# Kernel optimization log

Measured on AMD Instinct MI355X. Metric: run time of the kernel, lower is better.

The kernel has to match this reference:

```python
import jax, jax.numpy as jnp
import numpy as np

B, T, D, H = 4, 256, 256, 4
D2 = 2 * D
DH = D2 // H
SCALE = float(D) ** -0.5


def _swish(x):
    return x * jax.nn.sigmoid(x)


def setup_inputs():
    key = jax.random.key(0)
    ks = jax.random.split(key, 16)

    def w(k, shape, fan_in):
        return jax.random.normal(k, shape, dtype=jnp.float32) / np.float32(np.sqrt(fan_in))

    return {
        "x": jax.random.normal(ks[0], (B, T, D), dtype=jnp.float32),
        "ln_g": jnp.ones((D,), jnp.float32), "ln_b": jnp.zeros((D,), jnp.float32),
        "W_left": w(ks[1], (D2, D), D), "b_left": jnp.zeros((D2,), jnp.float32),
        "W_right": w(ks[2], (D2, D), D), "b_right": jnp.zeros((D2,), jnp.float32),
        "Wi": w(ks[3], (1, D2), D2), "bi": jnp.zeros((1,), jnp.float32),
        "Wf": w(ks[4], (1, D2), D2), "bf": jnp.zeros((1,), jnp.float32),
        "Wo": w(ks[5], (D2, D2), D2), "bo": jnp.zeros((D2,), jnp.float32),
        "Wq": w(ks[6], (H, DH, DH), DH),
        "Wk": w(ks[7], (H, DH, DH), DH),
        "Wv": w(ks[8], (H, DH, DH), DH),
        "conv_w": w(ks[9], (D2, D2, 4), D2 * 4), "conv_b": jnp.zeros((D2,), jnp.float32),
        "skip_W": w(ks[10], (D2, D2), D2),
        "gn_g": jnp.ones((D2,), jnp.float32), "gn_b": jnp.zeros((D2,), jnp.float32),
        "W_last": w(ks[11], (D, D2), D2), "b_last": jnp.zeros((D,), jnp.float32),
    }


def reference(x, ln_g, ln_b, W_left, b_left, W_right, b_right, Wi, bi, Wf, bf,
              Wo, bo, Wq, Wk, Wv, conv_w, conv_b, skip_W, gn_g, gn_b, W_last, b_last):
    # LayerNorm over last dim (eps=1e-5, torch default)
    mu = x.mean(-1, keepdims=True)
    var = x.var(-1, keepdims=True)
    x_norm = (x - mu) * jax.lax.rsqrt(var + 1e-5) * ln_g + ln_b

    x_left = x_norm @ W_left.T + b_left          # (B,T,D2)
    x_right = x_norm @ W_right.T + b_right       # (B,T,D2)

    # causal conv1d: kernel 4, left pad 3
    xc = jnp.transpose(x_left, (0, 2, 1))        # (B,C,T)
    yc = jax.lax.conv_general_dilated(xc, conv_w, (1,), [(3, 0)],
                                      dimension_numbers=("NCH", "OIH", "NCH"))
    x_trans = _swish(jnp.transpose(yc + conv_b[None, :, None], (0, 2, 1)))  # (B,T,D2)

    def bd(z, W):  # block-diagonal linear, W: (H, out_h, in_h)
        zr = z.reshape(B, T, H, DH)
        return jnp.einsum("bthi,hoi->btho", zr, W).reshape(B, T, D2)

    # precompute all per-step projections (hoist GEMMs out of the scan)
    i_bar = x_left @ Wi.T + bi                   # (B,T,1)
    f_bar = x_left @ Wf.T + bf                   # (B,T,1)
    o = jax.nn.sigmoid(x_left @ Wo.T + bo)       # (B,T,D2)
    q = bd(x_trans, Wq)
    k = SCALE * bd(x_trans, Wk)
    v = bd(x_left, Wv)

    xs = tuple(jnp.swapaxes(a, 0, 1) for a in (i_bar, f_bar, q, k, v))  # (T,B,...)
    c0 = jnp.zeros((B, D2, D2), x.dtype)
    n0 = jnp.zeros((B, D2), x.dtype)
    m0 = jnp.zeros((B, 1), x.dtype)

    def step(carry, xs_t):
        c, n, m = carry
        ib, fb, qt, kt, vt = xs_t
        m_next = jnp.maximum(fb + m, ib)
        i_g = jnp.exp(ib - m_next)               # (B,1)
        f_g = jnp.exp(fb + m - m_next)           # (B,1)
        c_next = f_g[..., None] * c + i_g[..., None] * (vt[:, :, None] * kt[:, None, :])
        n_next = f_g * n + i_g * kt
        cq = jnp.einsum("bde,be->bd", c_next, qt)
        denom = jnp.maximum(jnp.abs(jnp.sum(n_next * qt, -1, keepdims=True)), 1.0)
        return (c_next, n_next, m_next), cq / (denom + 1e-8)

    _, h_bar = jax.lax.scan(step, (c0, n0, m0), xs)
    h_seq = o * jnp.swapaxes(h_bar, 0, 1)        # (B,T,D2), output gate applied per step

    # GroupNorm on (B, C, T): normalize per (batch, group) over C/G and T
    z = h_seq.reshape(B, T, H, DH)
    mu_g = z.mean(axis=(1, 3), keepdims=True)
    var_g = z.var(axis=(1, 3), keepdims=True)
    zn = ((z - mu_g) * jax.lax.rsqrt(var_g + 1e-5)).reshape(B, T, D2)
    h_gn = zn * gn_g + gn_b + x_trans @ skip_W.T

    h = h_gn * _swish(x_right)
    return h @ W_last.T + b_last + x
```

## Files before the change

kernel.cpp:

```cpp
#include <hip/hip_runtime.h>
#include <hip/hip_bf16.h>
#include <cstdint>

#define Bz 4
#define Tz 256
#define Dz 256
#define D2z 512
#define Hz 4
#define DHz 128
#define BT (Bz*Tz)

__device__ __forceinline__ float dot4(float4 a, float4 b){
  return a.x*b.x + a.y*b.y + a.z*b.z + a.w*b.w;
}
__device__ __forceinline__ float sigmoidf_(float z){ return 1.f/(1.f+__expf(-z)); }
__device__ __forceinline__ float4 fma4(float4 a, float4 w, float s){
  a.x += w.x*s; a.y += w.y*s; a.z += w.z*s; a.w += w.w*s; return a;
}
__device__ __forceinline__ float4 add4(float4 a, float4 b){
  a.x+=b.x; a.y+=b.y; a.z+=b.z; a.w+=b.w; return a;
}

__global__ void __launch_bounds__(256) k_tr(
    const float* __restrict__ Wo, const float* __restrict__ SW,
    const float* __restrict__ Wl, const float* __restrict__ Wq,
    const float* __restrict__ Wk, const float* __restrict__ Wv,
    const float* __restrict__ CW,
    float* __restrict__ Wot, float* __restrict__ SWt, float* __restrict__ WLt,
    float* __restrict__ Wqt, float* __restrict__ Wkt, float* __restrict__ Wvt,
    float* __restrict__ CWt){
  int bid = blockIdx.x, tid = threadIdx.x;
  if (bid < 208){
    __shared__ float ts[64][65];
    const float* src; float* dst; int O,K,to,tk;
    if (bid<64){ src=Wo; dst=Wot; O=512;K=512; to=bid>>3; tk=bid&7; }
    else if (bid<128){ int r=bid-64; src=SW; dst=SWt; O=512;K=512; to=r>>3; tk=r&7; }
    else if (bid<160){ int r=bid-128; src=Wl; dst=WLt; O=256;K=512; to=r>>3; tk=r&7; }
    else {
      int r=bid-160; int m=r>>4; int rr=r&15; int h=rr>>2; int s=rr&3;
      src=(m==0?Wq:m==1?Wk:Wv) + h*16384;
      dst=(m==0?Wqt:m==1?Wkt:Wvt) + h*16384;
      O=128; K=128; to=s>>1; tk=s&1;
    }
    int lk=tid&63, ro=tid>>6;
    #pragma unroll
    for(int p=0;p<16;p++) ts[p*4+ro][lk] = src[(size_t)(to*64+p*4+ro)*K + tk*64+lk];
    __syncthreads();
    #pragma unroll
    for(int p=0;p<16;p++) dst[(size_t)(tk*64+p*4+ro)*O + to*64+lk] = ts[lk][p*4+ro];
  } else {
    __shared__ float4 t4[32][33];
    int r = bid-208; int to=r>>4, tk=r&15;
    const float4* src4=(const float4*)CW; float4* dst4=(float4*)CWt;
    int li=tid&31, ro=tid>>5;
    #pragma unroll
    for(int p=0;p<4;p++) t4[p*8+ro][li] = src4[(size_t)(to*32+p*8+ro)*512 + tk*32+li];
    __syncthreads();
    #pragma unroll
    for(int p=0;p<4;p++) dst4[(size_t)(tk*32+p*8+ro)*512 + to*32+li] = t4[li][p*8+ro];
  }
}

__global__ void __launch_bounds__(512,2) k_lnlr(
    const float* __restrict__ x, const float* __restrict__ lg,
    const float* __restrict__ lb, const float* __restrict__ WL,
    const float* __restrict__ bL, const float* __restrict__ WR,
    const float* __restrict__ bR,
    const float* __restrict__ Wi, const float* __restrict__ bi,
    const float* __restrict__ Wf, const float* __restrict__ bf,
    float* __restrict__ xl, float* __restrict__ xr,
    float* __restrict__ ibp, float* __restrict__ fbp){
  __shared__ float xs[8][Dz];
  __shared__ float rif[2][4][8];
  int r0 = blockIdx.x*8; int oh = blockIdx.y;
  int tid = threadIdx.x;
  ((float4*)&xs[0][0])[tid] = ((const float4*)(x + (size_t)r0*Dz))[tid];
  __syncthreads();
  int w = tid>>6, lane = tid&63;
  float a0 = xs[w][lane],     a1 = xs[w][lane+64];
  float a2 = xs[w][lane+128], a3 = xs[w][lane+192];
  float s  = a0+a1+a2+a3;
  float s2 = a0*a0+a1*a1+a2*a2+a3*a3;
  #pragma unroll
  for (int off=1; off<64; off<<=1){ s += __shfl_xor(s, off); s2 += __shfl_xor(s2, off); }
  float mu = s*(1.f/Dz);
  float rs = rsqrtf(s2*(1.f/Dz)-mu*mu+1e-5f);
  xs[w][lane]     = (a0-mu)*rs*lg[lane]    +lb[lane];
  xs[w][lane+64]  = (a1-mu)*rs*lg[lane+64] +lb[lane+64];
  xs[w][lane+128] = (a2-mu)*rs*lg[lane+128]+lb[lane+128];
  xs[w][lane+192] = (a3-mu)*rs*lg[lane+192]+lb[lane+192];
  __syncthreads();
  int which = tid>>8;
  int o = oh*256 + (tid&255);
  float acc[8]={0,0,0,0,0,0,0,0};
  const float* WM = which ? WR : WL;
  const float4* wm4 = (const float4*)(WM + (size_t)o*Dz);
  #pragma unroll 2
  for (int k4=0;k4<Dz/4;k4++){
    float4 wv=wm4[k4];
    #pragma unroll
    for(int tt=0;tt<8;tt++) acc[tt] += dot4(wv, ((const float4*)xs[tt])[k4]);
  }
  if (which==0){
    float blv=bL[o], wi_o=Wi[o], wf_o=Wf[o];
    float pi[8], pf[8];
    #pragma unroll
    for(int tt=0;tt<8;tt++){
      float xlv = acc[tt]+blv;
      xl[(size_t)(r0+tt)*D2z+o]=xlv;
      pi[tt]=xlv*wi_o; pf[tt]=xlv*wf_o;
    }
    #pragma unroll
    for(int off=1;off<64;off<<=1){
      #pragma unroll
      for(int tt=0;tt<8;tt++){ pi[tt]+=__shfl_xor(pi[tt],off); pf[tt]+=__shfl_xor(pf[tt],off); }
    }
    if(lane==0){
      #pragma unroll
      for(int tt=0;tt<8;tt++){ rif[0][w][tt]=pi[tt]; rif[1][w][tt]=pf[tt]; }
    }
  } else {
    float brv=bR[o];
    #pragma unroll
    for(int tt=0;tt<8;tt++) xr[(size_t)(r0+tt)*D2z+o]=acc[tt]+brv;
  }
  __syncthreads();
  if(tid<16){
    int r=tid&7, which2=tid>>3;
    float sv=0.f;
    #pragma unroll
    for(int ww=0;ww<4;ww++) sv+=rif[which2][ww][r];
    float bias = (oh==0) ? (which2==0 ? bi[0] : bf[0]) : 0.f;
    (which2==0 ? ibp : fbp)[oh*BT + r0 + r] = sv + bias;
  }
}

__global__ void __launch_bounds__(256,2) k_mid(
    const float* __restrict__ xl, const float* __restrict__ CWt,
    const float* __restrict__ cb, float* __restrict__ xt,
    const float* __restrict__ Wot, const float* __restrict__ bo,
    const float* __restrict__ Wvt, float* __restrict__ og, float* __restrict__ vv,
    const float* __restrict__ ibp, const float* __restrict__ fbp,
    float* __restrict__ G, float* __restrict__ Mx){
  __shared__ __align__(16) float smem[14080];
  int bid = blockIdx.x, tid = threadIdx.x;
  if (bid < 512){
    float (*xs)[D2z] = (float(*)[D2z])smem;
    float (*red)[64][17] = (float(*)[64][17])(smem + 19*D2z);
    int tile = bid&63, o0 = (bid>>6)*64;
    int b = tile>>4; int t0 = (tile&15)*16;
    for(int idx=tid; idx<19*(D2z/4); idx+=256){
      int j = idx>>7, k4 = idx&127;
      int t = t0-3+j;
      float4 v = (t>=0) ? ((const float4*)(xl + (size_t)((b<<8)+t)*D2z))[k4]
                        : make_float4(0.f,0.f,0.f,0.f);
      ((float4*)xs[j])[k4]=v;
    }
    __syncthreads();
    int ol = tid&63, ch = tid>>6;
    int o = o0 + ol, ic0 = ch*128;
    float acc[16];
    #pragma unroll
    for(int tt=0;tt<16;tt++) acc[tt]=0.f;
    const float4* w4 = (const float4*)CWt + o;
    for(int i=0;i<128;i+=4){
      int ig = ic0+i;
      float4 w0=w4[(size_t)(ig+0)*512], w1=w4[(size_t)(ig+1)*512];
      float4 w2=w4[(size_t)(ig+2)*512], w3=w4[(size_t)(ig+3)*512];
      float4 xr4[19];
      #pragma unroll
      for(int j=0;j<19;j++) xr4[j]=*(const float4*)&xs[j][ig];
      #pragma unroll
      for(int tt=0;tt<16;tt++){
        acc[tt] += w0.x*xr4[tt].x + w0.y*xr4[tt+1].x + w0.z*xr4[tt+2].x + w0.w*xr4[tt+3].x
                 + w1.x*xr4[tt].y + w1.y*xr4[tt+1].y + w1.z*xr4[tt+2].y + w1.w*xr4[tt+3].y
                 + w2.x*xr4[tt].z + w2.y*xr4[tt+1].z + w2.z*xr4[tt+2].z + w2.w*xr4[tt+3].z
                 + w3.x*xr4[tt].w + w3.y*xr4[tt+1].w + w3.z*xr4[tt+2].w + w3.w*xr4[tt+3].w;
      }
    }
    #pragma unroll
    for(int tt=0;tt<16;tt++) red[ch][ol][tt]=acc[tt];
    __syncthreads();
    for(int idx=tid; idx<1024; idx+=256){
      int oo = idx&63, t = idx>>6;
      float y = red[0][oo][t]+red[1][oo][t]+red[2][oo][t]+red[3][oo][t] + cb[o0+oo];
      xt[(size_t)((b<<8)+t0+t)*D2z + o0+oo] = y*sigmoidf_(y);
    }
  } else if (bid < 1024){
    float (*xs)[D2z] = (float(*)[D2z])smem;
    float4 (*ored)[4][64] = (float4(*)[4][64])(smem + 4*D2z);
    float4 (*vred)[4][64] = (float4(*)[4][64])(smem + 4*D2z + 4096);
    int wbid = bid-512;
    int r0=(wbid&255)*4; int oh=wbid>>8;
    for(int idx=tid;idx<512;idx+=256)
      ((float4*)&xs[0][0])[idx]=((const float4*)(xl+(size_t)r0*D2z))[idx];
    __syncthreads();
    int ol=tid&63, ch=tid>>6;
    float4 a0={0,0,0,0},a1={0,0,0,0},a2={0,0,0,0},a3={0,0,0,0};
    const float4* wp=(const float4*)Wot + (size_t)ch*16384 + (oh*64+ol);
    #pragma unroll 2
    for(int kq=0;kq<32;kq++){
      int k=ch*128+kq*4;
      float4 w0=wp[(kq*4+0)*128], w1=wp[(kq*4+1)*128], w2=wp[(kq*4+2)*128], w3=wp[(kq*4+3)*128];
      float4 x0=*(const float4*)&xs[0][k];
      float4 x1=*(const float4*)&xs[1][k];
      float4 x2=*(const float4*)&xs[2][k];
      float4 x3=*(const float4*)&xs[3][k];
      a0=fma4(fma4(fma4(fma4(a0,w0,x0.x),w1,x0.y),w2,x0.z),w3,x0.w);
      a1=fma4(fma4(fma4(fma4(a1,w0,x1.x),w1,x1.y),w2,x1.z),w3,x1.w);
      a2=fma4(fma4(fma4(fma4(a2,w0,x2.x),w1,x2.y),w2,x2.z),w3,x2.w);
      a3=fma4(fma4(fma4(fma4(a3,w0,x3.x),w1,x3.y),w2,x3.z),w3,x3.w);
    }
    ored[ch][0][ol]=a0; ored[ch][1][ol]=a1; ored[ch][2][ol]=a2; ored[ch][3][ol]=a3;
    {
      int h = oh*2 + (ol>>5), odq = ol&31;
      float4 v0={0,0,0,0},v1={0,0,0,0},v2={0,0,0,0},v3={0,0,0,0};
      const float4* wv=(const float4*)Wvt + (size_t)h*4096 + (size_t)(ch*32)*32 + odq;
      int xoff = h*128 + ch*32;
      #pragma unroll 2
      for(int iq=0;iq<8;iq++){
        float4 w0=wv[(iq*4+0)*32], w1=wv[(iq*4+1)*32], w2=wv[(iq*4+2)*32], w3=wv[(iq*4+3)*32];
        float4 x0=*(const float4*)&xs[0][xoff+iq*4];
        float4 x1=*(const float4*)&xs[1][xoff+iq*4];
        float4 x2=*(const float4*)&xs[2][xoff+iq*4];
        float4 x3=*(const float4*)&xs[3][xoff+iq*4];
        v0=fma4(fma4(fma4(fma4(v0,w0,x0.x),w1,x0.y),w2,x0.z),w3,x0.w);
        v1=fma4(fma4(fma4(fma4(v1,w0,x1.x),w1,x1.y),w2,x1.z),w3,x1.w);
        v2=fma4(fma4(fma4(fma4(v2,w0,x2.x),w1,x2.y),w2,x2.z),w3,x2.w);
        v3=fma4(fma4(fma4(fma4(v3,w0,x3.x),w1,x3.y),w2,x3.z),w3,x3.w);
      }
      vred[ch][0][ol]=v0; vred[ch][1][ol]=v1; vred[ch][2][ol]=v2; vred[ch][3][ol]=v3;
    }
    __syncthreads();
    int tt=tid>>6, oo=tid&63;
    float4 s=add4(add4(ored[0][tt][oo],ored[1][tt][oo]),add4(ored[2][tt][oo],ored[3][tt][oo]));
    float4 bb=((const float4*)bo)[oh*64+oo];
    s.x=sigmoidf_(s.x+bb.x); s.y=sigmoidf_(s.y+bb.y);
    s.z=sigmoidf_(s.z+bb.z); s.w=sigmoidf_(s.w+bb.w);
    float4 vs=add4(add4(vred[0][tt][oo],vred[1][tt][oo]),add4(vred[2][tt][oo],vred[3][tt][oo]));
    size_t row=r0+tt;
    ((float4*)(og+row*D2z))[oh*64+oo]=s;
    ((float4*)(vv+row*D2z))[oh*64+oo]=vs;
  } else {
    float* buf = smem;
    int b = bid-1024, t = tid;
    float f = fbp[b*Tz + t] + fbp[BT + b*Tz + t];
    float ibv = ibp[b*Tz + t] + ibp[BT + b*Tz + t];
    buf[t] = f; __syncthreads();
    float v = f;
    for (int off=1; off<Tz; off<<=1){
      float add = (t >= off) ? buf[t-off] : 0.f;
      __syncthreads();
      v += add; buf[t] = v;
      __syncthreads();
    }
    float F = v;
    float g = ibv - F;
    G[b*Tz+t] = g;
    buf[t] = g; __syncthreads();
    v = g;
    for (int off=1; off<Tz; off<<=1){
      float other = (t >= off) ? buf[t-off] : -3.4e38f;
      __syncthreads();
      v = fmaxf(v, other); buf[t] = v;
      __syncthreads();
    }
    Mx[b*Tz+t] = fmaxf(v, 0.f);
  }
}

__global__ void __launch_bounds__(256,2) k_qks(const float* __restrict__ xt,
    const float* __restrict__ SWt, const float* __restrict__ Wqt,
    const float* __restrict__ Wkt,
    float* __restrict__ qq, float* __restrict__ kk, float* __restrict__ sk){
  __shared__ float xs[4][D2z];
  __shared__ float4 sred[4][4][64];
  __shared__ float4 qred[4][4][64];
  __shared__ float4 kred[4][4][64];
  int r0=blockIdx.x*4; int oh=blockIdx.y; int tid=threadIdx.x;
  for(int idx=tid;idx<512;idx+=256)
    ((float4*)&xs[0][0])[idx]=((const float4*)(xt+(size_t)r0*D2z))[idx];
  __syncthreads();
  int ol=tid&63, ch=tid>>6;
  float4 s0={0,0,0,0},s1={0,0,0,0},s2={0,0,0,0},s3={0,0,0,0};
  const float4* wp=(const float4*)SWt + (size_t)ch*16384 + (oh*64+ol);
  #pragma unroll 2
  for(int kq=0;kq<32;kq++){
    int k=ch*128+kq*4;
    float4 w0=wp[(kq*4+0)*128], w1=wp[(kq*4+1)*128], w2=wp[(kq*4+2)*128], w3=wp[(kq*4+3)*128];
    float4 x0=*(const float4*)&xs[0][k];
    float4 x1=*(const float4*)&xs[1][k];
    float4 x2=*(const float4*)&xs[2][k];
    float4 x3=*(const float4*)&xs[3][k];
    s0=fma4(fma4(fma4(fma4(s0,w0,x0.x),w1,x0.y),w2,x0.z),w3,x0.w);
    s1=fma4(fma4(fma4(fma4(s1,w0,x1.x),w1,x1.y),w2,x1.z),w3,x1.w);
    s2=fma4(fma4(fma4(fma4(s2,w0,x2.x),w1,x2.y),w2,x2.z),w3,x2.w);
    s3=fma4(fma4(fma4(fma4(s3,w0,x3.x),w1,x3.y),w2,x3.z),w3,x3.w);
  }
  sred[ch][0][ol]=s0; sred[ch][1][ol]=s1; sred[ch][2][ol]=s2; sred[ch][3][ol]=s3;
  {
    int h = oh*2 + (ol>>5), odq = ol&31;
    float4 q0={0,0,0,0},q1={0,0,0,0},q2={0,0,0,0},q3={0,0,0,0};
    float4 c0={0,0,0,0},c1={0,0,0,0},c2={0,0,0,0},c3={0,0,0,0};
    const float4* wq=(const float4*)Wqt + (size_t)h*4096 + (size_t)(ch*32)*32 + odq;
    const float4* wk=(const float4*)Wkt + (size_t)h*4096 + (size_t)(ch*32)*32 + odq;
    int xoff = h*128 + ch*32;
    #pragma unroll 2
    for(int iq=0;iq<8;iq++){
      float4 qa0=wq[(iq*4+0)*32], qa1=wq[(iq*4+1)*32], qa2=wq[(iq*4+2)*32], qa3=wq[(iq*4+3)*32];
      float4 ka0=wk[(iq*4+0)*32], ka1=wk[(iq*4+1)*32], ka2=wk[(iq*4+2)*32], ka3=wk[(iq*4+3)*32];
      float4 x0=*(const float4*)&xs[0][xoff+iq*4];
      float4 x1=*(const float4*)&xs[1][xoff+iq*4];
      float4 x2=*(const float4*)&xs[2][xoff+iq*4];
      float4 x3=*(const float4*)&xs[3][xoff+iq*4];
      q0=fma4(fma4(fma4(fma4(q0,qa0,x0.x),qa1,x0.y),qa2,x0.z),qa3,x0.w);
      q1=fma4(fma4(fma4(fma4(q1,qa0,x1.x),qa1,x1.y),qa2,x1.z),qa3,x1.w);
      q2=fma4(fma4(fma4(fma4(q2,qa0,x2.x),qa1,x2.y),qa2,x2.z),qa3,x2.w);
      q3=fma4(fma4(fma4(fma4(q3,qa0,x3.x),qa1,x3.y),qa2,x3.z),qa3,x3.w);
      c0=fma4(fma4(fma4(fma4(c0,ka0,x0.x),ka1,x0.y),ka2,x0.z),ka3,x0.w);
      c1=fma4(fma4(fma4(fma4(c1,ka0,x1.x),ka1,x1.y),ka2,x1.z),ka3,x1.w);
      c2=fma4(fma4(fma4(fma4(c2,ka0,x2.x),ka1,x2.y),ka2,x2.z),ka3,x2.w);
      c3=fma4(fma4(fma4(fma4(c3,ka0,x3.x),ka1,x3.y),ka2,x3.z),ka3,x3.w);
    }
    qred[ch][0][ol]=q0; qred[ch][1][ol]=q1; qred[ch][2][ol]=q2; qred[ch][3][ol]=q3;
    kred[ch][0][ol]=c0; kred[ch][1][ol]=c1; kred[ch][2][ol]=c2; kred[ch][3][ol]=c3;
  }
  __syncthreads();
  int tt=tid>>6, oo=tid&63;
  float4 sv=add4(add4(sred[0][tt][oo],sred[1][tt][oo]),add4(sred[2][tt][oo],sred[3][tt][oo]));
  float4 qv=add4(add4(qred[0][tt][oo],qred[1][tt][oo]),add4(qred[2][tt][oo],qred[3][tt][oo]));
  float4 kv=add4(add4(kred[0][tt][oo],kred[1][tt][oo]),add4(kred[2][tt][oo],kred[3][tt][oo]));
  kv.x*=0.0625f; kv.y*=0.0625f; kv.z*=0.0625f; kv.w*=0.0625f;
  size_t row=r0+tt;
  ((float4*)(sk+row*D2z))[oh*64+oo]=sv;
  ((float4*)(qq+row*D2z))[oh*64+oo]=qv;
  ((float4*)(kk+row*D2z))[oh*64+oo]=kv;
}

#define TTa 4
__global__ void __launch_bounds__(256) k_attn(
    const float* __restrict__ qq, const float* __restrict__ kk,
    const float* __restrict__ vv, const float* __restrict__ og,
    const float* __restrict__ G, const float* __restrict__ Mx,
    float* __restrict__ hs){
  int b  = blockIdx.y;
  int t0 = blockIdx.x * TTa;
  int tid = threadIdx.x;
  __shared__ float Qs[TTa][D2z];
  __shared__ float Ps[TTa][Tz];
  __shared__ float Gs[Tz];
  __shared__ float inv_d[TTa];
  __shared__ float mxs[TTa];

  const float* qb = qq + ((size_t)b*Tz + t0)*D2z;
  for (int idx=tid; idx<TTa*D2z/4; idx+=256)
    ((float4*)&Qs[0][0])[idx] = ((const float4*)qb)[idx];
  Gs[tid] = G[b*Tz + tid];
  if (tid < TTa) mxs[tid] = Mx[b*Tz + t0 + tid];
  __syncthreads();

  int s = tid;
  int smax = t0 + TTa - 1;
  {
    float acc[TTa] = {0,0,0,0};
    if (s <= smax){
      const float4* kp = (const float4*)(kk + ((size_t)b*Tz + s)*D2z);
      for (int k4=0; k4<D2z/4; k4++){
        float4 kv = kp[k4];
        #pragma unroll
        for (int tt=0; tt<TTa; tt++){
          float4 qv = ((const float4*)Qs[tt])[k4];
          acc[tt] += dot4(kv,qv);
        }
      }
    }
    float g = Gs[s];
    #pragma unroll
    for (int tt=0; tt<TTa; tt++){
      int t = t0 + tt;
      Ps[tt][s] = (s <= t) ? acc[tt] * __expf(g - mxs[tt]) : 0.f;
    }
  }
  __syncthreads();
  {
    int wv = tid >> 6, lane = tid & 63;
    int tt = wv;
    float ssum = Ps[tt][lane] + Ps[tt][lane+64] + Ps[tt][lane+128] + Ps[tt][lane+192];
    #pragma unroll
    for (int off=1; off<64; off<<=1) ssum += __shfl_xor(ssum, off);
    if (lane==0) inv_d[tt] = 1.f / (fmaxf(fabsf(ssum), 1.f) + 1e-8f);
  }
  __syncthreads();
  {
    int c0 = tid, c1 = tid + 256;
    float a0[TTa]={0,0,0,0}, a1[TTa]={0,0,0,0};
    const float* vb = vv + (size_t)b*Tz*D2z;
    for (int s2=0; s2<=smax; s2+=4){
      float4 pr[TTa];
      #pragma unroll
      for (int tt=0; tt<TTa; tt++) pr[tt] = *(const float4*)&Ps[tt][s2];
      #pragma unroll
      for (int j=0; j<4; j++){
        int sj = s2 + j;
        float v0 = vb[(size_t)sj*D2z + c0];
        float v1 = vb[(size_t)sj*D2z + c1];
        #pragma unroll
        for (int tt=0; tt<TTa; tt++){
          float p = ((const float*)&pr[tt])[j];
          a0[tt] += p*v0; a1[tt] += p*v1;
        }
      }
    }
    #pragma unroll
    for (int tt=0; tt<TTa; tt++){
      size_t row = (size_t)b*Tz + t0 + tt;
      float id = inv_d[tt];
      hs[row*D2z + c0] = og[row*D2z + c0] * a0[tt] * id;
      hs[row*D2z + c1] = og[row*D2z + c1] * a1[tt] * id;
    }
  }
}

__global__ void k_gnstat(const float* __restrict__ hs,float* __restrict__ gmu,
                         float* __restrict__ grs){
  int g=blockIdx.x; int b=g>>2,h=g&3; int tid=threadIdx.x;
  float s=0.f,s2=0.f;
  const float* base=hs+(size_t)b*Tz*D2z+h*DHz;
  for(int idx=tid;idx<Tz*DHz;idx+=256){
    int t=idx>>7,c=idx&127;
    float v=base[(size_t)t*D2z+c];
    s+=v;s2+=v*v;
  }
  #pragma unroll
  for(int off=32;off;off>>=1){s+=__shfl_down(s,off);s2+=__shfl_down(s2,off);}
  __shared__ float ls[8];
  int wid=tid>>6,lane=tid&63;
  if(lane==0){ls[wid]=s;ls[4+wid]=s2;}
  __syncthreads();
  if(tid==0){
    float S=ls[0]+ls[1]+ls[2]+ls[3],S2=ls[4]+ls[5]+ls[6]+ls[7];
    float mu=S*(1.f/(Tz*DHz));
    float var=S2*(1.f/(Tz*DHz))-mu*mu;
    gmu[g]=mu; grs[g]=rsqrtf(fmaxf(var,0.f)+1e-5f);
  }
}

__global__ void __launch_bounds__(512,2) k_final(const float* __restrict__ hs,
    const float* __restrict__ gmu, const float* __restrict__ grs,
    const float* __restrict__ gng, const float* __restrict__ gnb,
    const float* __restrict__ sk, const float* __restrict__ xr,
    const float* __restrict__ WLt, const float* __restrict__ bl,
    const float* __restrict__ x, float* __restrict__ out){
  __shared__ float hm[4][D2z];
  __shared__ float4 red[8][4][64];
  int r0=blockIdx.x*4; int b=r0>>8; int tid=threadIdx.x;
  for(int idx=tid;idx<4*D2z;idx+=512){
    int tt=idx>>9,c=idx&511;
    size_t row=r0+tt;
    int g=(b<<2)+(c>>7);
    float v=hs[row*D2z+c];
    float hg=(v-gmu[g])*grs[g]*gng[c]+gnb[c]+sk[row*D2z+c];
    float xv=xr[row*D2z+c];
    hm[tt][c]=hg*(xv*sigmoidf_(xv));
  }
  __syncthreads();
  int ol=tid&63, ch=tid>>6;
  float4 a0={0,0,0,0},a1={0,0,0,0},a2={0,0,0,0},a3={0,0,0,0};
  const float4* wp=(const float4*)WLt + (size_t)(ch*64)*64 + ol;
  #pragma unroll 2
  for(int kq=0;kq<16;kq++){
    int k=ch*64+kq*4;
    float4 w0=wp[(kq*4+0)*64], w1=wp[(kq*4+1)*64], w2=wp[(kq*4+2)*64], w3=wp[(kq*4+3)*64];
    float4 x0=*(const float4*)&hm[0][k];
    float4 x1=*(const float4*)&hm[1][k];
    float4 x2=*(const float4*)&hm[2][k];
    float4 x3=*(const float4*)&hm[3][k];
    a0=fma4(fma4(fma4(fma4(a0,w0,x0.x),w1,x0.y),w2,x0.z),w3,x0.w);
    a1=fma4(fma4(fma4(fma4(a1,w0,x1.x),w1,x1.y),w2,x1.z),w3,x1.w);
    a2=fma4(fma4(fma4(fma4(a2,w0,x2.x),w1,x2.y),w2,x2.z),w3,x2.w);
    a3=fma4(fma4(fma4(fma4(a3,w0,x3.x),w1,x3.y),w2,x3.z),w3,x3.w);
  }
  red[ch][0][ol]=a0; red[ch][1][ol]=a1; red[ch][2][ol]=a2; red[ch][3][ol]=a3;
  __syncthreads();
  if(tid<256){
    int tt=tid>>6, oo=tid&63;
    float4 sv={0,0,0,0};
    #pragma unroll
    for(int c2=0;c2<8;c2++) sv=add4(sv,red[c2][tt][oo]);
    float4 bb=((const float4*)bl)[oo];
    float4 xv=((const float4*)(x+(size_t)(r0+tt)*Dz))[oo];
    sv.x+=bb.x+xv.x; sv.y+=bb.y+xv.y; sv.z+=bb.z+xv.z; sv.w+=bb.w+xv.w;
    ((float4*)(out+(size_t)(r0+tt)*Dz))[oo]=sv;
  }
}

extern "C" void kernel_launch(void* const* d_in, const int* in_sizes, int n_in,
                              void* d_out, int out_size, void* d_ws, size_t ws_size,
                              hipStream_t stream) {
  (void)in_sizes; (void)n_in; (void)out_size; (void)ws_size;
  const float* x      = (const float*)d_in[0];
  const float* ln_g   = (const float*)d_in[1];
  const float* ln_b   = (const float*)d_in[2];
  const float* W_left = (const float*)d_in[3];
  const float* b_left = (const float*)d_in[4];
  const float* W_right= (const float*)d_in[5];
  const float* b_right= (const float*)d_in[6];
  const float* Wi     = (const float*)d_in[7];
  const float* bi     = (const float*)d_in[8];
  const float* Wf     = (const float*)d_in[9];
  const float* bf     = (const float*)d_in[10];
  const float* Wo     = (const float*)d_in[11];
  const float* bo     = (const float*)d_in[12];
  const float* Wq     = (const float*)d_in[13];
  const float* Wk     = (const float*)d_in[14];
  const float* Wv     = (const float*)d_in[15];
  const float* conv_w = (const float*)d_in[16];
  const float* conv_b = (const float*)d_in[17];
  const float* skip_W = (const float*)d_in[18];
  const float* gn_g   = (const float*)d_in[19];
  const float* gn_b   = (const float*)d_in[20];
  const float* W_last = (const float*)d_in[21];
  const float* b_last = (const float*)d_in[22];
  float* out = (float*)d_out;

  float* ws = (float*)d_ws;
  float* Wot  = ws;
  float* xl   = ws + 262144;
  float* xr   = ws + 786432;
  float* xt   = ws + 1310720;
  float* og   = ws + 1835008;
  float* vv   = ws + 2359296;
  float* qq   = ws + 2883584;
  float* kk   = ws + 3407872;
  float* sk   = ws + 3932160;
  float* hs   = ws + 4456448;
  float* ibp  = ws + 4980736;
  float* fbp  = ws + 4982784;
  float* gmu  = ws + 4984832;
  float* grs  = ws + 4984848;
  float* Gd   = ws + 4984864;
  float* Mxd  = ws + 4985888;
  float* SWt  = ws + 4986912;
  float* WLt  = ws + 5249056;
  float* Wqt  = ws + 5380128;
  float* Wkt  = ws + 5445664;
  float* Wvt  = ws + 5511200;
  float* CWt  = ws + 5576736;

  k_tr    <<<464, 256, 0, stream>>>(Wo, skip_W, W_last, Wq, Wk, Wv, conv_w,
                                    Wot, SWt, WLt, Wqt, Wkt, Wvt, CWt);
  k_lnlr  <<<dim3(BT/8, 2), 512, 0, stream>>>(x, ln_g, ln_b, W_left, b_left, W_right, b_right,
                                              Wi, bi, Wf, bf, xl, xr, ibp, fbp);
  k_mid   <<<1028, 256, 0, stream>>>(xl, CWt, conv_b, xt, Wot, bo, Wvt, og, vv,
                                     ibp, fbp, Gd, Mxd);
  k_qks   <<<dim3(BT/4, 2), 256, 0, stream>>>(xt, SWt, Wqt, Wkt, qq, kk, sk);
  k_attn  <<<dim3(Tz/TTa, Bz), 256, 0, stream>>>(qq, kk, vv, og, Gd, Mxd, hs);
  k_gnstat<<<Bz*Hz, 256, 0, stream>>>(hs, gmu, grs);
  k_final <<<BT/4, 512, 0, stream>>>(hs, gmu, grs, gn_g, gn_b, sk, xr, WLt, b_last, x, out);
}
```

Measured before the change: 186.2 us.

## Merge weight transpose with LayerNorm projections and fuse GroupNorm stats into attention

Merges the weight-transpose kernel and the LayerNorm/left-right projection kernel into one 512-thread launch. It also drops the separate GroupNorm statistics kernel: the attention kernel now accumulates per-group sums and sums of squares with atomics, and the final kernel derives mean and rstd from them. k_mid reuses its input shared buffer for the reduction, which shrinks shared memory and raises launch bounds to 4 blocks per CU. The aim is fewer launches, no extra pass over hs and better occupancy. The costs are float atomics, with nondeterministic summation order, and a gsum zeroing that relies on stream ordering.

```diff
diff --git a/kernel.cpp b/kernel.cpp
--- a/kernel.cpp
+++ b/kernel.cpp
@@ -21,17 +21,28 @@
   a.x+=b.x; a.y+=b.y; a.z+=b.z; a.w+=b.w; return a;
 }
 
-__global__ void __launch_bounds__(256) k_tr(
+__global__ void __launch_bounds__(512,2) k_pre(
     const float* __restrict__ Wo, const float* __restrict__ SW,
     const float* __restrict__ Wl, const float* __restrict__ Wq,
     const float* __restrict__ Wk, const float* __restrict__ Wv,
     const float* __restrict__ CW,
     float* __restrict__ Wot, float* __restrict__ SWt, float* __restrict__ WLt,
     float* __restrict__ Wqt, float* __restrict__ Wkt, float* __restrict__ Wvt,
-    float* __restrict__ CWt){
+    float* __restrict__ CWt,
+    const float* __restrict__ x, const float* __restrict__ lg,
+    const float* __restrict__ lb, const float* __restrict__ WL,
+    const float* __restrict__ bL, const float* __restrict__ WR,
+    const float* __restrict__ bR,
+    const float* __restrict__ Wi, const float* __restrict__ bi,
+    const float* __restrict__ Wf, const float* __restrict__ bf,
+    float* __restrict__ xl, float* __restrict__ xr,
+    float* __restrict__ ibp, float* __restrict__ fbp,
+    float* __restrict__ gsum){
+  __shared__ __align__(16) float smem[4224];
   int bid = blockIdx.x, tid = threadIdx.x;
   if (bid < 208){
-    __shared__ float ts[64][65];
+    if (bid==0 && tid<32) gsum[tid]=0.f;
+    float (*ts)[65] = (float(*)[65])smem;
     const float* src; float* dst; int O,K,to,tk;
     if (bid<64){ src=Wo; dst=Wot; O=512;K=512; to=bid>>3; tk=bid&7; }
     else if (bid<128){ int r=bid-64; src=SW; dst=SWt; O=512;K=512; to=r>>3; tk=r&7; }
@@ -44,109 +55,98 @@
     }
     int lk=tid&63, ro=tid>>6;
     #pragma unroll
-    for(int p=0;p<16;p++) ts[p*4+ro][lk] = src[(size_t)(to*64+p*4+ro)*K + tk*64+lk];
-    __syncthreads();
-    #pragma unroll
-    for(int p=0;p<16;p++) dst[(size_t)(tk*64+p*4+ro)*O + to*64+lk] = ts[lk][p*4+ro];
-  } else {
-    __shared__ float4 t4[32][33];
+    for(int p=0;p<8;p++) ts[p*8+ro][lk] = src[(size_t)(to*64+p*8+ro)*K + tk*64+lk];
+    __syncthreads();
+    #pragma unroll
+    for(int p=0;p<8;p++) dst[(size_t)(tk*64+p*8+ro)*O + to*64+lk] = ts[lk][p*8+ro];
+  } else if (bid < 464){
+    float4 (*t4)[33] = (float4(*)[33])smem;
     int r = bid-208; int to=r>>4, tk=r&15;
     const float4* src4=(const float4*)CW; float4* dst4=(float4*)CWt;
     int li=tid&31, ro=tid>>5;
     #pragma unroll
-    for(int p=0;p<4;p++) t4[p*8+ro][li] = src4[(size_t)(to*32+p*8+ro)*512 + tk*32+li];
-    __syncthreads();
-    #pragma unroll
-    for(int p=0;p<4;p++) dst4[(size_t)(tk*32+p*8+ro)*512 + to*32+li] = t4[li][p*8+ro];
-  }
-}
-
-__global__ void __launch_bounds__(512,2) k_lnlr(
-    const float* __restrict__ x, const float* __restrict__ lg,
-    const float* __restrict__ lb, const float* __restrict__ WL,
-    const float* __restrict__ bL, const float* __restrict__ WR,
-    const float* __restrict__ bR,
-    const float* __restrict__ Wi, const float* __restrict__ bi,
-    const float* __restrict__ Wf, const float* __restrict__ bf,
-    float* __restrict__ xl, float* __restrict__ xr,
-    float* __restrict__ ibp, float* __restrict__ fbp){
-  __shared__ float xs[8][Dz];
-  __shared__ float rif[2][4][8];
-  int r0 = blockIdx.x*8; int oh = blockIdx.y;
-  int tid = threadIdx.x;
-  ((float4*)&xs[0][0])[tid] = ((const float4*)(x + (size_t)r0*Dz))[tid];
-  __syncthreads();
-  int w = tid>>6, lane = tid&63;
-  float a0 = xs[w][lane],     a1 = xs[w][lane+64];
-  float a2 = xs[w][lane+128], a3 = xs[w][lane+192];
-  float s  = a0+a1+a2+a3;
-  float s2 = a0*a0+a1*a1+a2*a2+a3*a3;
-  #pragma unroll
-  for (int off=1; off<64; off<<=1){ s += __shfl_xor(s, off); s2 += __shfl_xor(s2, off); }
-  float mu = s*(1.f/Dz);
-  float rs = rsqrtf(s2*(1.f/Dz)-mu*mu+1e-5f);
-  xs[w][lane]     = (a0-mu)*rs*lg[lane]    +lb[lane];
-  xs[w][lane+64]  = (a1-mu)*rs*lg[lane+64] +lb[lane+64];
-  xs[w][lane+128] = (a2-mu)*rs*lg[lane+128]+lb[lane+128];
-  xs[w][lane+192] = (a3-mu)*rs*lg[lane+192]+lb[lane+192];
-  __syncthreads();
-  int which = tid>>8;
-  int o = oh*256 + (tid&255);
-  float acc[8]={0,0,0,0,0,0,0,0};
-  const float* WM = which ? WR : WL;
-  const float4* wm4 = (const float4*)(WM + (size_t)o*Dz);
-  #pragma unroll 2
-  for (int k4=0;k4<Dz/4;k4++){
-    float4 wv=wm4[k4];
-    #pragma unroll
-    for(int tt=0;tt<8;tt++) acc[tt] += dot4(wv, ((const float4*)xs[tt])[k4]);
-  }
-  if (which==0){
-    float blv=bL[o], wi_o=Wi[o], wf_o=Wf[o];
-    float pi[8], pf[8];
-    #pragma unroll
-    for(int tt=0;tt<8;tt++){
-      float xlv = acc[tt]+blv;
-      xl[(size_t)(r0+tt)*D2z+o]=xlv;
-      pi[tt]=xlv*wi_o; pf[tt]=xlv*wf_o;
-    }
-    #pragma unroll
-    for(int off=1;off<64;off<<=1){
-      #pragma unroll
-      for(int tt=0;tt<8;tt++){ pi[tt]+=__shfl_xor(pi[tt],off); pf[tt]+=__shfl_xor(pf[tt],off); }
-    }
-    if(lane==0){
-      #pragma unroll
-      for(int tt=0;tt<8;tt++){ rif[0][w][tt]=pi[tt]; rif[1][w][tt]=pf[tt]; }
-    }
+    for(int p=0;p<2;p++) t4[p*16+ro][li] = src4[(size_t)(to*32+p*16+ro)*512 + tk*32+li];
+    __syncthreads();
+    #pragma unroll
+    for(int p=0;p<2;p++) dst4[(size_t)(tk*32+p*16+ro)*512 + to*32+li] = t4[li][p*16+ro];
   } else {
-    float brv=bR[o];
-    #pragma unroll
-    for(int tt=0;tt<8;tt++) xr[(size_t)(r0+tt)*D2z+o]=acc[tt]+brv;
-  }
-  __syncthreads();
-  if(tid<16){
-    int r=tid&7, which2=tid>>3;
-    float sv=0.f;
-    #pragma unroll
-    for(int ww=0;ww<4;ww++) sv+=rif[which2][ww][r];
-    float bias = (oh==0) ? (which2==0 ? bi[0] : bf[0]) : 0.f;
-    (which2==0 ? ibp : fbp)[oh*BT + r0 + r] = sv + bias;
-  }
-}
-
-__global__ void __launch_bounds__(256,2) k_mid(
+    float (*xs)[Dz] = (float(*)[Dz])smem;
+    float (*rif)[4][8] = (float(*)[4][8])(smem + 8*Dz);
+    int wbid = bid-464;
+    int r0 = (wbid&127)*8; int oh = wbid>>7;
+    ((float4*)&xs[0][0])[tid] = ((const float4*)(x + (size_t)r0*Dz))[tid];
+    __syncthreads();
+    int w = tid>>6, lane = tid&63;
+    float a0 = xs[w][lane],     a1 = xs[w][lane+64];
+    float a2 = xs[w][lane+128], a3 = xs[w][lane+192];
+    float s  = a0+a1+a2+a3;
+    float s2 = a0*a0+a1*a1+a2*a2+a3*a3;
+    #pragma unroll
+    for (int off=1; off<64; off<<=1){ s += __shfl_xor(s, off); s2 += __shfl_xor(s2, off); }
+    float mu = s*(1.f/Dz);
+    float rs = rsqrtf(s2*(1.f/Dz)-mu*mu+1e-5f);
+    xs[w][lane]     = (a0-mu)*rs*lg[lane]    +lb[lane];
+    xs[w][lane+64]  = (a1-mu)*rs*lg[lane+64] +lb[lane+64];
+    xs[w][lane+128] = (a2-mu)*rs*lg[lane+128]+lb[lane+128];
+    xs[w][lane+192] = (a3-mu)*rs*lg[lane+192]+lb[lane+192];
+    __syncthreads();
+    int which = tid>>8;
+    int o = oh*256 + (tid&255);
+    float acc[8]={0,0,0,0,0,0,0,0};
+    const float* WM = which ? WR : WL;
+    const float4* wm4 = (const float4*)(WM + (size_t)o*Dz);
+    #pragma unroll 2
+    for (int k4=0;k4<Dz/4;k4++){
+      float4 wv=wm4[k4];
+      #pragma unroll
+      for(int tt=0;tt<8;tt++) acc[tt] += dot4(wv, ((const float4*)xs[tt])[k4]);
+    }
+    if (which==0){
+      float blv=bL[o], wi_o=Wi[o], wf_o=Wf[o];
+      float pi[8], pf[8];
+      #pragma unroll
+      for(int tt=0;tt<8;tt++){
+        float xlv = acc[tt]+blv;
+        xl[(size_t)(r0+tt)*D2z+o]=xlv;
+        pi[tt]=xlv*wi_o; pf[tt]=xlv*wf_o;
+      }
+      #pragma unroll
+      for(int off=1;off<64;off<<=1){
+        #pragma unroll
+        for(int tt=0;tt<8;tt++){ pi[tt]+=__shfl_xor(pi[tt],off); pf[tt]+=__shfl_xor(pf[tt],off); }
+      }
+      if(lane==0){
+        #pragma unroll
+        for(int tt=0;tt<8;tt++){ rif[0][w][tt]=pi[tt]; rif[1][w][tt]=pf[tt]; }
+      }
+    } else {
+      float brv=bR[o];
+      #pragma unroll
+      for(int tt=0;tt<8;tt++) xr[(size_t)(r0+tt)*D2z+o]=acc[tt]+brv;
+    }
+    __syncthreads();
+    if(tid<16){
+      int r=tid&7, which2=tid>>3;
+      float sv=0.f;
+      #pragma unroll
+      for(int ww=0;ww<4;ww++) sv+=rif[which2][ww][r];
+      float bias = (oh==0) ? (which2==0 ? bi[0] : bf[0]) : 0.f;
+      (which2==0 ? ibp : fbp)[oh*BT + r0 + r] = sv + bias;
+    }
+  }
+}
+
+__global__ void __launch_bounds__(256,4) k_mid(
     const float* __restrict__ xl, const float* __restrict__ CWt,
     const float* __restrict__ cb, float* __restrict__ xt,
     const float* __restrict__ Wot, const float* __restrict__ bo,
     const float* __restrict__ Wvt, float* __restrict__ og, float* __restrict__ vv,
     const float* __restrict__ ibp, const float* __restrict__ fbp,
     float* __restrict__ G, float* __restrict__ Mx){
-  __shared__ __align__(16) float smem[14080];
+  __shared__ __align__(16) float smem[10240];
   int bid = blockIdx.x, tid = threadIdx.x;
   if (bid < 512){
     float (*xs)[D2z] = (float(*)[D2z])smem;
-    float (*red)[64][17] = (float(*)[64][17])(smem + 19*D2z);
     int tile = bid&63, o0 = (bid>>6)*64;
     int b = tile>>4; int t0 = (tile&15)*16;
     for(int idx=tid; idx<19*(D2z/4); idx+=256){
@@ -178,6 +178,8 @@
                  + w3.x*xr4[tt].w + w3.y*xr4[tt+1].w + w3.z*xr4[tt+2].w + w3.w*xr4[tt+3].w;
       }
     }
+    __syncthreads();
+    float (*red)[64][17] = (float(*)[64][17])smem;
     #pragma unroll
     for(int tt=0;tt<16;tt++) red[ch][ol][tt]=acc[tt];
     __syncthreads();
@@ -342,7 +344,7 @@
     const float* __restrict__ qq, const float* __restrict__ kk,
     const float* __restrict__ vv, const float* __restrict__ og,
     const float* __restrict__ G, const float* __restrict__ Mx,
-    float* __restrict__ hs){
+    float* __restrict__ hs, float* __restrict__ gsum){
   int b  = blockIdx.y;
   int t0 = blockIdx.x * TTa;
   int tid = threadIdx.x;
@@ -411,42 +413,32 @@
         }
       }
     }
+    float s0=0.f,q0=0.f,s1=0.f,q1=0.f;
     #pragma unroll
     for (int tt=0; tt<TTa; tt++){
       size_t row = (size_t)b*Tz + t0 + tt;
       float id = inv_d[tt];
-      hs[row*D2z + c0] = og[row*D2z + c0] * a0[tt] * id;
-      hs[row*D2z + c1] = og[row*D2z + c1] * a1[tt] * id;
-    }
-  }
-}
-
-__global__ void k_gnstat(const float* __restrict__ hs,float* __restrict__ gmu,
-                         float* __restrict__ grs){
-  int g=blockIdx.x; int b=g>>2,h=g&3; int tid=threadIdx.x;
-  float s=0.f,s2=0.f;
-  const float* base=hs+(size_t)b*Tz*D2z+h*DHz;
-  for(int idx=tid;idx<Tz*DHz;idx+=256){
-    int t=idx>>7,c=idx&127;
-    float v=base[(size_t)t*D2z+c];
-    s+=v;s2+=v*v;
-  }
-  #pragma unroll
-  for(int off=32;off;off>>=1){s+=__shfl_down(s,off);s2+=__shfl_down(s2,off);}
-  __shared__ float ls[8];
-  int wid=tid>>6,lane=tid&63;
-  if(lane==0){ls[wid]=s;ls[4+wid]=s2;}
-  __syncthreads();
-  if(tid==0){
-    float S=ls[0]+ls[1]+ls[2]+ls[3],S2=ls[4]+ls[5]+ls[6]+ls[7];
-    float mu=S*(1.f/(Tz*DHz));
-    float var=S2*(1.f/(Tz*DHz))-mu*mu;
-    gmu[g]=mu; grs[g]=rsqrtf(fmaxf(var,0.f)+1e-5f);
+      float h0 = og[row*D2z + c0] * a0[tt] * id;
+      float h1 = og[row*D2z + c1] * a1[tt] * id;
+      hs[row*D2z + c0] = h0;
+      hs[row*D2z + c1] = h1;
+      s0+=h0; q0+=h0*h0; s1+=h1; q1+=h1*h1;
+    }
+    #pragma unroll
+    for (int off=1; off<64; off<<=1){
+      s0+=__shfl_xor(s0,off); q0+=__shfl_xor(q0,off);
+      s1+=__shfl_xor(s1,off); q1+=__shfl_xor(q1,off);
+    }
+    if ((tid&63)==0){
+      int g0=(b<<2)+(c0>>7), g1=(b<<2)+(c1>>7);
+      atomicAdd(&gsum[g0], s0);    atomicAdd(&gsum[16+g0], q0);
+      atomicAdd(&gsum[g1], s1);    atomicAdd(&gsum[16+g1], q1);
+    }
   }
 }
 
 __global__ void __launch_bounds__(512,2) k_final(const float* __restrict__ hs,
-    const float* __restrict__ gmu, const float* __restrict__ grs,
+    const float* __restrict__ gsum,
     const float* __restrict__ gng, const float* __restrict__ gnb,
     const float* __restrict__ sk, const float* __restrict__ xr,
     const float* __restrict__ WLt, const float* __restrict__ bl,
@@ -458,8 +450,12 @@
     int tt=idx>>9,c=idx&511;
     size_t row=r0+tt;
     int g=(b<<2)+(c>>7);
+    float S=gsum[g], S2=gsum[16+g];
+    float mu=S*(1.f/(Tz*DHz));
+    float var=S2*(1.f/(Tz*DHz))-mu*mu;
+    float rs=rsqrtf(fmaxf(var,0.f)+1e-5f);
     float v=hs[row*D2z+c];
-    float hg=(v-gmu[g])*grs[g]*gng[c]+gnb[c]+sk[row*D2z+c];
+    float hg=(v-mu)*rs*gng[c]+gnb[c]+sk[row*D2z+c];
     float xv=xr[row*D2z+c];
     hm[tt][c]=hg*(xv*sigmoidf_(xv));
   }
@@ -536,8 +532,7 @@
   float* hs   = ws + 4456448;
   float* ibp  = ws + 4980736;
   float* fbp  = ws + 4982784;
-  float* gmu  = ws + 4984832;
-  float* grs  = ws + 4984848;
+  float* gsum = ws + 4984832;
   float* Gd   = ws + 4984864;
   float* Mxd  = ws + 4985888;
   float* SWt  = ws + 4986912;
@@ -547,14 +542,13 @@
   float* Wvt  = ws + 5511200;
   float* CWt  = ws + 5576736;
 
-  k_tr    <<<464, 256, 0, stream>>>(Wo, skip_W, W_last, Wq, Wk, Wv, conv_w,
-                                    Wot, SWt, WLt, Wqt, Wkt, Wvt, CWt);
-  k_lnlr  <<<dim3(BT/8, 2), 512, 0, stream>>>(x, ln_g, ln_b, W_left, b_left, W_right, b_right,
-                                              Wi, bi, Wf, bf, xl, xr, ibp, fbp);
+  k_pre   <<<720, 512, 0, stream>>>(Wo, skip_W, W_last, Wq, Wk, Wv, conv_w,
+                                    Wot, SWt, WLt, Wqt, Wkt, Wvt, CWt,
+                                    x, ln_g, ln_b, W_left, b_left, W_right, b_right,
+                                    Wi, bi, Wf, bf, xl, xr, ibp, fbp, gsum);
   k_mid   <<<1028, 256, 0, stream>>>(xl, CWt, conv_b, xt, Wot, bo, Wvt, og, vv,
                                      ibp, fbp, Gd, Mxd);
   k_qks   <<<dim3(BT/4, 2), 256, 0, stream>>>(xt, SWt, Wqt, Wkt, qq, kk, sk);
-  k_attn  <<<dim3(Tz/TTa, Bz), 256, 0, stream>>>(qq, kk, vv, og, Gd, Mxd, hs);
-  k_gnstat<<<Bz*Hz, 256, 0, stream>>>(hs, gmu, grs);
-  k_final <<<BT/4, 512, 0, stream>>>(hs, gmu, grs, gn_g, gn_b, sk, xr, WLt, b_last, x, out);
-}
+  k_attn  <<<dim3(Tz/TTa, Bz), 256, 0, stream>>>(qq, kk, vv, og, Gd, Mxd, hs, gsum);
+  k_final <<<BT/4, 512, 0, stream>>>(hs, gsum, gn_g, gn_b, sk, xr, WLt, b_last, x, out);
+}
```

Result: slower. 213.3 us (+14.5%).
